# Kernel tuning notes

Hardware: AMD Instinct MI355X
Metric: run time of the kernel (lower is better)

The kernel has to match this reference:

```python
import jax, jax.numpy as jnp
import numpy as np
from jax import lax


def setup_inputs() -> dict:
    key = jax.random.key(0)
    k1, k2 = jax.random.split(key)
    L, B, d = 2048, 16, 1024
    x = jax.random.normal(k1, (L, B, d), dtype=jnp.float32)
    val_range = (3.0 / d) ** 0.5
    weight = jax.random.uniform(k2, (d, 3 * d), dtype=jnp.float32,
                                minval=-val_range, maxval=val_range)
    bias = jnp.zeros((2 * d,), dtype=jnp.float32)
    c0 = jnp.zeros((B, d), dtype=jnp.float32)
    return {"x": x, "weight": weight, "bias": bias, "c0": c0}


def reference(x, weight, bias, c0):
    # x: [L, B, d]; weight: [d, 3d]; bias: [2d]; c0: [B, d]
    L, B, d = x.shape
    u = (x.reshape(-1, d) @ weight).reshape(L, B, d, 3)
    x_tilde = u[..., 0]                               # [L, B, d]
    forget = jax.nn.sigmoid(u[..., 1] + bias[:d])     # [L, B, d]
    reset = jax.nn.sigmoid(u[..., 2] + bias[d:])      # [L, B, d]
    # k == 3 case: x_prime is the raw input (highway connection)
    x_prime = x

    def step(c_prev, ft_xt):
        ft, xt = ft_xt
        c = (c_prev - xt) * ft + xt
        return c, c

    c_last, cs = lax.scan(step, c0, (forget, x_tilde))
    g = jnp.tanh(cs)  # activation_type == 1
    h = (g - x_prime) * reset + x_prime
    return h, c_last
```

## Files before the change

### kernel.cpp

```cpp
#include <hip/hip_runtime.h>

#define L_SEQ 2048
#define BATCH 16
#define DDIM  1024
#define MDIM  (L_SEQ * BATCH)
#define NDIM  (3 * DDIM)
#define KDIM  DDIM
#define CH    (BATCH * DDIM)
#define NSEG  32
#define SEGL  64

typedef __attribute__((ext_vector_type(8))) short short8;
typedef __attribute__((ext_vector_type(4))) float f32x4;

static __device__ __forceinline__ unsigned short f2bf(float f) {
  unsigned int u = __builtin_bit_cast(unsigned int, f);
  unsigned int lsb = (u >> 16) & 1u;
  u += 0x7fffu + lsb;
  return (unsigned short)(u >> 16);
}
static __device__ __forceinline__ float bf2f(unsigned short s) {
  unsigned int u = ((unsigned int)s) << 16;
  return __builtin_bit_cast(float, u);
}

static __device__ __forceinline__ void gll16(const void* g, void* l) {
  __builtin_amdgcn_global_load_lds(
      (const __attribute__((address_space(1))) unsigned int*)g,
      (__attribute__((address_space(3))) unsigned int*)l, 16, 0, 0);
}


__global__ void k_convert_x(const float4* __restrict__ x, ushort4* __restrict__ xb, int n4) {
  int i = blockIdx.x * blockDim.x + threadIdx.x;
  int stride = gridDim.x * blockDim.x;
  for (; i < n4; i += stride) {
    float4 v = x[i];
    ushort4 o;
    o.x = f2bf(v.x); o.y = f2bf(v.y); o.z = f2bf(v.z); o.w = f2bf(v.w);
    xb[i] = o;
  }
}

__global__ void k_convert_w(const float* __restrict__ w, unsigned short* __restrict__ wb) {
  int gid = blockIdx.x * 256 + threadIdx.x;
  int k = gid & (KDIM - 1);
  int n = gid >> 10;
  int col = (n < DDIM) ? 3 * n : (n < 2 * DDIM) ? 3 * (n - DDIM) + 1 : 3 * (n - 2 * DDIM) + 2;
  wb[gid] = f2bf(w[(size_t)k * NDIM + col]);
}


#define MFMA1(I, J, A, B) \
  acc[I][J] = __builtin_amdgcn_mfma_f32_16x16x32_bf16(A, B, acc[I][J], 0, 0, 0);

#define TILE32(T) do {                                                        \
  const char* bufC = LDSc + ((T) & 1) * 16384;                                \
  char*       bufN = LDSc + (((T) + 1) & 1) * 16384;                          \
  const int kb = (((T) + 1) & 31) * 64;                                       \
  gll16(srcA0 + kb, bufN + dstOff);                                           \
  gll16(srcA1 + kb, bufN + 4096 + dstOff);                                    \
  gll16(srcB0 + kb, bufN + 8192 + dstOff);                                    \
  gll16(srcB1 + kb, bufN + 12288 + dstOff);                                   \
  __builtin_amdgcn_sched_barrier(0);                                          \
  a0 = *(const short8*)(bufC + aRd);                                          \
  a1 = *(const short8*)(bufC + aRd + 1024);                                   \
  a2 = *(const short8*)(bufC + aRd + 2048);                                   \
  a3 = *(const short8*)(bufC + aRd + 3072);                                   \
  b0 = *(const short8*)(bufC + 8192 + bRd);                                   \
  b1 = *(const short8*)(bufC + 8192 + bRd + 1024);                            \
  b2 = *(const short8*)(bufC + 8192 + bRd + 2048);                            \
  b3 = *(const short8*)(bufC + 8192 + bRd + 3072);                            \
  MFMA1(0, 0, a0, b0) MFMA1(0, 1, a0, b1) MFMA1(0, 2, a0, b2) MFMA1(0, 3, a0, b3) \
  MFMA1(1, 0, a1, b0) MFMA1(1, 1, a1, b1) MFMA1(1, 2, a1, b2) MFMA1(1, 3, a1, b3) \
  MFMA1(2, 0, a2, b0) MFMA1(2, 1, a2, b1) MFMA1(2, 2, a2, b2) MFMA1(2, 3, a2, b3) \
  MFMA1(3, 0, a3, b0) MFMA1(3, 1, a3, b1) MFMA1(3, 2, a3, b2) MFMA1(3, 3, a3, b3) \
  asm volatile("s_waitcnt vmcnt(0)" ::: "memory");                            \
  __builtin_amdgcn_s_barrier();                                               \
} while (0)

__global__ __launch_bounds__(256, 3) void k_gemm128(
    const unsigned short* __restrict__ xb,
    const unsigned short* __restrict__ wb,
    const float* __restrict__ bias,
    unsigned short* __restrict__ xtb,
    unsigned short* __restrict__ fbuf,
    unsigned short* __restrict__ rbuf) {
  __shared__ char LDS[32768];
  char* LDSc = LDS;

  const int tid  = threadIdx.x;
  const int lane = tid & 63;
  const int wid  = tid >> 6;
  const int wr   = wid >> 1;
  const int wc   = wid & 1;

  int bid = blockIdx.x;
  int wg = (bid & 7) * 768 + (bid >> 3);
  int mt = wg / 24;
  int nt = wg - mt * 24;
  const int rowBase = mt * 128;
  const int colBase = nt * 128;

  const int l15 = lane & 15;
  const int sl  = lane >> 4;
  const int ra0 = wr * 64 + l15;
  const int rb0 = wc * 64 + l15;
  const int aRd = ra0 * 64 + (sl ^ ((ra0 >> 1) & 3)) * 16;
  const int bRd = rb0 * 64 + (sl ^ ((rb0 >> 1) & 3)) * 16;

  const int p0i = tid, p1i = 256 + tid;
  const int r0 = p0i >> 2, r1 = p1i >> 2;
  const int s0 = (p0i & 3) ^ ((r0 >> 1) & 3);
  const int s1 = (p1i & 3) ^ ((r1 >> 1) & 3);
  const char* srcA0 = (const char*)xb + (size_t)(rowBase + r0) * 2048 + s0 * 16;
  const char* srcA1 = (const char*)xb + (size_t)(rowBase + r1) * 2048 + s1 * 16;
  const char* srcB0 = (const char*)wb + (size_t)(colBase + r0) * 2048 + s0 * 16;
  const char* srcB1 = (const char*)wb + (size_t)(colBase + r1) * 2048 + s1 * 16;
  const int dstOff = wid * 1024;

  f32x4 acc[4][4];
#pragma unroll
  for (int ii = 0; ii < 4; ++ii)
#pragma unroll
    for (int jj = 0; jj < 4; ++jj)
      acc[ii][jj] = (f32x4){0.f, 0.f, 0.f, 0.f};

  gll16(srcA0, LDSc + dstOff);
  gll16(srcA1, LDSc + 4096 + dstOff);
  gll16(srcB0, LDSc + 8192 + dstOff);
  gll16(srcB1, LDSc + 12288 + dstOff);
  asm volatile("s_waitcnt vmcnt(0)" ::: "memory");
  __builtin_amdgcn_s_barrier();

  short8 a0, a1, a2, a3;
  short8 b0, b1, b2, b3;

  for (int i = 0; i < 16; ++i) {
    TILE32(2 * i);
    TILE32(2 * i + 1);
  }

  const int region = colBase >> 10;
#pragma unroll
  for (int m = 0; m < 4; ++m) {
    int grow = rowBase + wr * 64 + m * 16 + ((lane >> 4) << 2);
#pragma unroll
    for (int n = 0; n < 4; ++n) {
      int gcol = colBase + wc * 64 + n * 16 + (lane & 15);
      f32x4 v = acc[m][n];
      if (region == 0) {
#pragma unroll
        for (int j = 0; j < 4; ++j)
          xtb[(size_t)(grow + j) * DDIM + gcol] = f2bf(v[j]);
      } else {
        float bv = bias[gcol - DDIM];
        unsigned short* dst = (region == 1) ? fbuf : rbuf;
        int lcol = gcol - (region << 10);
#pragma unroll
        for (int j = 0; j < 4; ++j) {
          float sg = 1.0f / (1.0f + __expf(-(v[j] + bv)));
          dst[(size_t)(grow + j) * DDIM + lcol] = f2bf(sg);
        }
      }
    }
  }
}


__global__ __launch_bounds__(256) void k_scan1(
    const unsigned short* __restrict__ fbuf,
    const unsigned short* __restrict__ xtb,
    float4* __restrict__ AB) {
  int chp = blockIdx.x * 256 + threadIdx.x;
  int seg = blockIdx.y;
  size_t base = (size_t)seg * SEGL * CH + chp * 2;
  const unsigned int* fp = (const unsigned int*)(fbuf + base);
  const unsigned int* xp = (const unsigned int*)(xtb + base);
  float a0 = 1.f, a1 = 1.f, b0 = 0.f, b1 = 0.f;
#pragma unroll 8
  for (int s = 0; s < SEGL; ++s) {
    unsigned int fv = fp[(size_t)s * (CH / 2)];
    unsigned int xv = xp[(size_t)s * (CH / 2)];
    float f0 = bf2f((unsigned short)fv), f1 = bf2f((unsigned short)(fv >> 16));
    float x0 = bf2f((unsigned short)xv), x1 = bf2f((unsigned short)(xv >> 16));
    b0 = (b0 - x0) * f0 + x0;  a0 *= f0;
    b1 = (b1 - x1) * f1 + x1;  a1 *= f1;
  }
  AB[(size_t)seg * (CH / 2) + chp] = (float4){a0, b0, a1, b1};
}


__global__ __launch_bounds__(256) void k_scan2(
    const float* __restrict__ c0,
    const float4* __restrict__ AB,
    float* __restrict__ Cin,
    float* __restrict__ clast) {
  int chp = blockIdx.x * 256 + threadIdx.x;
  float2 cc = ((const float2*)c0)[chp];
  float ca = cc.x, cb = cc.y;
#pragma unroll
  for (int s = 0; s < NSEG; ++s) {
    ((float2*)Cin)[(size_t)s * (CH / 2) + chp] = (float2){ca, cb};
    float4 ab = AB[(size_t)s * (CH / 2) + chp];
    ca = ca * ab.x + ab.y;
    cb = cb * ab.z + ab.w;
  }
  ((float2*)clast)[chp] = (float2){ca, cb};
}


__global__ __launch_bounds__(256) void k_scan3(
    const float* __restrict__ x,
    const unsigned short* __restrict__ fbuf,
    const unsigned short* __restrict__ xtb,
    const unsigned short* __restrict__ rbuf,
    const float* __restrict__ Cin,
    float* __restrict__ h) {
  int chp = blockIdx.x * 256 + threadIdx.x;
  int seg = blockIdx.y;
  float2 cc = ((const float2*)Cin)[(size_t)seg * (CH / 2) + chp];
  float ca = cc.x, cb = cc.y;
  size_t base = (size_t)seg * SEGL * CH + chp * 2;
  const unsigned int* fp = (const unsigned int*)(fbuf + base);
  const unsigned int* tp = (const unsigned int*)(xtb + base);
  const unsigned int* rp = (const unsigned int*)(rbuf + base);
  const float2* xp = (const float2*)(x + base);
  float2* hp = (float2*)(h + base);
#pragma unroll 4
  for (int s = 0; s < SEGL; ++s) {
    unsigned int fv = fp[(size_t)s * (CH / 2)];
    unsigned int tv = tp[(size_t)s * (CH / 2)];
    unsigned int rv = rp[(size_t)s * (CH / 2)];
    float2 xv = xp[(size_t)s * (CH / 2)];
    float f0 = bf2f((unsigned short)fv), f1 = bf2f((unsigned short)(fv >> 16));
    float t0 = bf2f((unsigned short)tv), t1 = bf2f((unsigned short)(tv >> 16));
    float r0 = bf2f((unsigned short)rv), r1 = bf2f((unsigned short)(rv >> 16));
    ca = (ca - t0) * f0 + t0;
    cb = (cb - t1) * f1 + t1;
    float e0 = __expf(-2.f * fabsf(ca));
    float e1 = __expf(-2.f * fabsf(cb));
    float g0 = copysignf((1.f - e0) / (1.f + e0), ca);
    float g1 = copysignf((1.f - e1) / (1.f + e1), cb);
    float h0 = (g0 - xv.x) * r0 + xv.x;
    float h1 = (g1 - xv.y) * r1 + xv.y;
    hp[(size_t)s * (CH / 2)] = (float2){h0, h1};
  }
}


extern "C" void kernel_launch(void* const* d_in, const int* in_sizes, int n_in,
                              void* d_out, int out_size, void* d_ws, size_t ws_size,
                              hipStream_t stream) {
  const float* x    = (const float*)d_in[0];
  const float* w    = (const float*)d_in[1];
  const float* bias = (const float*)d_in[2];
  const float* c0   = (const float*)d_in[3];
  float* out = (float*)d_out;
  char* ws = (char*)d_ws;

  unsigned short* wb   = (unsigned short*)(ws);
  float4*         AB   = (float4*)(ws);
  float*          Cin  = (float*)(ws + 4194304);
  unsigned short* xtb  = (unsigned short*)(ws + 6291456);
  unsigned short* fbuf = (unsigned short*)(ws + 73400320);
  unsigned short* rbuf = (unsigned short*)(ws + 140509184);
  unsigned short* xb = (unsigned short*)d_out;

  k_convert_x<<<2048, 256, 0, stream>>>((const float4*)x, (ushort4*)xb, MDIM * KDIM / 4);
  k_convert_w<<<(NDIM * KDIM) / 256, 256, 0, stream>>>(w, wb);

  k_gemm128<<<6144, 256, 0, stream>>>(xb, wb, bias, xtb, fbuf, rbuf);

  k_scan1<<<dim3(32, NSEG), 256, 0, stream>>>(fbuf, xtb, AB);
  k_scan2<<<32, 256, 0, stream>>>(c0, AB, Cin, out + (size_t)L_SEQ * CH);
  k_scan3<<<dim3(32, NSEG), 256, 0, stream>>>(x, fbuf, xtb, rbuf, Cin, out);
}
```

Before: 463.1 us.

## Enlarge GEMM tile to 256x256 with 32x32 MFMA, quad-buffered LDS, and vectorize scans

Replaces the 128x128 GEMM tile (4 waves, 16x16x32 MFMA, double-buffered LDS) with a 256x256 tile using 8 waves, 32x32x16 MFMA, a 4-stage LDS ring with two K-steps prefetched ahead, and s_setprio around the MFMA block. Larger tiles raise arithmetic intensity and cut global and LDS traffic per FLOP, and the deeper prefetch hides load latency. The cost is 128KB of LDS per block and more registers, which lowers occupancy. The scan kernels now process 8 channels per thread with 16-byte loads, using fewer, wider memory transactions but fewer threads in flight.

```diff
diff --git a/kernel.cpp b/kernel.cpp
--- a/kernel.cpp
+++ b/kernel.cpp
@@ -12,6 +12,7 @@
 
 typedef __attribute__((ext_vector_type(8))) short short8;
 typedef __attribute__((ext_vector_type(4))) float f32x4;
+typedef __attribute__((ext_vector_type(16))) float f32x16;
 
 static __device__ __forceinline__ unsigned short f2bf(float f) {
   unsigned int u = __builtin_bit_cast(unsigned int, f);
@@ -51,116 +52,156 @@
 }
 
 
-#define MFMA1(I, J, A, B) \
-  acc[I][J] = __builtin_amdgcn_mfma_f32_16x16x32_bf16(A, B, acc[I][J], 0, 0, 0);
+#define MFMA32(ACC, A, B) \
+  ACC = __builtin_amdgcn_mfma_f32_32x32x16_bf16(A, B, ACC, 0, 0, 0);
 
 #define TILE32(T) do {                                                        \
-  const char* bufC = LDSc + ((T) & 1) * 16384;                                \
-  char*       bufN = LDSc + (((T) + 1) & 1) * 16384;                          \
-  const int kb = (((T) + 1) & 31) * 64;                                       \
-  gll16(srcA0 + kb, bufN + dstOff);                                           \
-  gll16(srcA1 + kb, bufN + 4096 + dstOff);                                    \
-  gll16(srcB0 + kb, bufN + 8192 + dstOff);                                    \
-  gll16(srcB1 + kb, bufN + 12288 + dstOff);                                   \
+  const char* bufC = LDSc + ((T) & 3) * 32768;                                \
+  char*       bufS = LDSc + (((T) + 2) & 3) * 32768;                          \
+  const int kb = (((T) + 2) & 31) * 64;                                       \
+  gll16(srcA0 + kb, bufS + dstOff);                                           \
+  gll16(srcA1 + kb, bufS + 8192 + dstOff);                                    \
+  gll16(srcB0 + kb, bufS + 16384 + dstOff);                                   \
+  gll16(srcB1 + kb, bufS + 24576 + dstOff);                                   \
   __builtin_amdgcn_sched_barrier(0);                                          \
-  a0 = *(const short8*)(bufC + aRd);                                          \
-  a1 = *(const short8*)(bufC + aRd + 1024);                                   \
-  a2 = *(const short8*)(bufC + aRd + 2048);                                   \
-  a3 = *(const short8*)(bufC + aRd + 3072);                                   \
-  b0 = *(const short8*)(bufC + 8192 + bRd);                                   \
-  b1 = *(const short8*)(bufC + 8192 + bRd + 1024);                            \
-  b2 = *(const short8*)(bufC + 8192 + bRd + 2048);                            \
-  b3 = *(const short8*)(bufC + 8192 + bRd + 3072);                            \
-  MFMA1(0, 0, a0, b0) MFMA1(0, 1, a0, b1) MFMA1(0, 2, a0, b2) MFMA1(0, 3, a0, b3) \
-  MFMA1(1, 0, a1, b0) MFMA1(1, 1, a1, b1) MFMA1(1, 2, a1, b2) MFMA1(1, 3, a1, b3) \
-  MFMA1(2, 0, a2, b0) MFMA1(2, 1, a2, b1) MFMA1(2, 2, a2, b2) MFMA1(2, 3, a2, b3) \
-  MFMA1(3, 0, a3, b0) MFMA1(3, 1, a3, b1) MFMA1(3, 2, a3, b2) MFMA1(3, 3, a3, b3) \
-  asm volatile("s_waitcnt vmcnt(0)" ::: "memory");                            \
+  fa0 = *(const short8*)(bufC + aA00);                                        \
+  fa1 = *(const short8*)(bufC + aA10);                                        \
+  fa2 = *(const short8*)(bufC + aA20);                                        \
+  fa3 = *(const short8*)(bufC + aA30);                                        \
+  fb0 = *(const short8*)(bufC + bA00);                                        \
+  fb1 = *(const short8*)(bufC + bA10);                                        \
+  ga0 = *(const short8*)(bufC + aA01);                                        \
+  ga1 = *(const short8*)(bufC + aA11);                                        \
+  ga2 = *(const short8*)(bufC + aA21);                                        \
+  ga3 = *(const short8*)(bufC + aA31);                                        \
+  gb0 = *(const short8*)(bufC + bA01);                                        \
+  gb1 = *(const short8*)(bufC + bA11);                                        \
+  __builtin_amdgcn_s_setprio(1);                                              \
+  MFMA32(acc[0][0], fa0, fb0) MFMA32(acc[0][1], fa0, fb1)                     \
+  MFMA32(acc[1][0], fa1, fb0) MFMA32(acc[1][1], fa1, fb1)                     \
+  MFMA32(acc[2][0], fa2, fb0) MFMA32(acc[2][1], fa2, fb1)                     \
+  MFMA32(acc[3][0], fa3, fb0) MFMA32(acc[3][1], fa3, fb1)                     \
+  MFMA32(acc[0][0], ga0, gb0) MFMA32(acc[0][1], ga0, gb1)                     \
+  MFMA32(acc[1][0], ga1, gb0) MFMA32(acc[1][1], ga1, gb1)                     \
+  MFMA32(acc[2][0], ga2, gb0) MFMA32(acc[2][1], ga2, gb1)                     \
+  MFMA32(acc[3][0], ga3, gb0) MFMA32(acc[3][1], ga3, gb1)                     \
+  __builtin_amdgcn_s_setprio(0);                                              \
+  asm volatile("s_waitcnt vmcnt(4)" ::: "memory");                            \
   __builtin_amdgcn_s_barrier();                                               \
 } while (0)
 
-__global__ __launch_bounds__(256, 3) void k_gemm128(
+__global__ __launch_bounds__(512, 2) void k_gemm256(
     const unsigned short* __restrict__ xb,
     const unsigned short* __restrict__ wb,
     const float* __restrict__ bias,
     unsigned short* __restrict__ xtb,
     unsigned short* __restrict__ fbuf,
     unsigned short* __restrict__ rbuf) {
-  __shared__ char LDS[32768];
+  __shared__ char LDS[131072];
   char* LDSc = LDS;
 
   const int tid  = threadIdx.x;
   const int lane = tid & 63;
   const int wid  = tid >> 6;
-  const int wr   = wid >> 1;
-  const int wc   = wid & 1;
+  const int wr   = wid >> 2;
+  const int wc   = wid & 3;
 
   int bid = blockIdx.x;
-  int wg = (bid & 7) * 768 + (bid >> 3);
-  int mt = wg / 24;
-  int nt = wg - mt * 24;
-  const int rowBase = mt * 128;
-  const int colBase = nt * 128;
-
-  const int l15 = lane & 15;
-  const int sl  = lane >> 4;
-  const int ra0 = wr * 64 + l15;
-  const int rb0 = wc * 64 + l15;
-  const int aRd = ra0 * 64 + (sl ^ ((ra0 >> 1) & 3)) * 16;
-  const int bRd = rb0 * 64 + (sl ^ ((rb0 >> 1) & 3)) * 16;
-
-  const int p0i = tid, p1i = 256 + tid;
-  const int r0 = p0i >> 2, r1 = p1i >> 2;
-  const int s0 = (p0i & 3) ^ ((r0 >> 1) & 3);
-  const int s1 = (p1i & 3) ^ ((r1 >> 1) & 3);
-  const char* srcA0 = (const char*)xb + (size_t)(rowBase + r0) * 2048 + s0 * 16;
-  const char* srcA1 = (const char*)xb + (size_t)(rowBase + r1) * 2048 + s1 * 16;
-  const char* srcB0 = (const char*)wb + (size_t)(colBase + r0) * 2048 + s0 * 16;
-  const char* srcB1 = (const char*)wb + (size_t)(colBase + r1) * 2048 + s1 * 16;
+  int wg = (bid & 7) * 192 + (bid >> 3);
+  int mt = wg / 12;
+  int nt = wg - mt * 12;
+  const int rowBase = mt * 256;
+  const int colBase = nt * 256;
+
+  const int l31 = lane & 31;
+  const int lh  = lane >> 5;
+  int aA00, aA10, aA20, aA30, aA01, aA11, aA21, aA31;
+  int bA00, bA10, bA01, bA11;
+  {
+    int r0 = wr * 128 + 0 * 32 + l31;
+    int r1 = wr * 128 + 1 * 32 + l31;
+    int r2 = wr * 128 + 2 * 32 + l31;
+    int r3 = wr * 128 + 3 * 32 + l31;
+    aA00 = r0 * 64 + (((lh + 0) ^ ((r0 >> 1) & 3)) << 4);
+    aA10 = r1 * 64 + (((lh + 0) ^ ((r1 >> 1) & 3)) << 4);
+    aA20 = r2 * 64 + (((lh + 0) ^ ((r2 >> 1) & 3)) << 4);
+    aA30 = r3 * 64 + (((lh + 0) ^ ((r3 >> 1) & 3)) << 4);
+    aA01 = r0 * 64 + (((lh + 2) ^ ((r0 >> 1) & 3)) << 4);
+    aA11 = r1 * 64 + (((lh + 2) ^ ((r1 >> 1) & 3)) << 4);
+    aA21 = r2 * 64 + (((lh + 2) ^ ((r2 >> 1) & 3)) << 4);
+    aA31 = r3 * 64 + (((lh + 2) ^ ((r3 >> 1) & 3)) << 4);
+    int c0 = wc * 64 + 0 * 32 + l31;
+    int c1 = wc * 64 + 1 * 32 + l31;
+    bA00 = 16384 + c0 * 64 + (((lh + 0) ^ ((c0 >> 1) & 3)) << 4);
+    bA10 = 16384 + c1 * 64 + (((lh + 0) ^ ((c1 >> 1) & 3)) << 4);
+    bA01 = 16384 + c0 * 64 + (((lh + 2) ^ ((c0 >> 1) & 3)) << 4);
+    bA11 = 16384 + c1 * 64 + (((lh + 2) ^ ((c1 >> 1) & 3)) << 4);
+  }
+
+  const int p0i = tid, p1i = 512 + tid;
+  const int r0s = p0i >> 2, r1s = p1i >> 2;
+  const int s0 = (p0i & 3) ^ ((r0s >> 1) & 3);
+  const int s1 = (p1i & 3) ^ ((r1s >> 1) & 3);
+  const char* srcA0 = (const char*)xb + (size_t)(rowBase + r0s) * 2048 + s0 * 16;
+  const char* srcA1 = (const char*)xb + (size_t)(rowBase + r1s) * 2048 + s1 * 16;
+  const char* srcB0 = (const char*)wb + (size_t)(colBase + r0s) * 2048 + s0 * 16;
+  const char* srcB1 = (const char*)wb + (size_t)(colBase + r1s) * 2048 + s1 * 16;
   const int dstOff = wid * 1024;
 
-  f32x4 acc[4][4];
+  f32x16 acc[4][2];
 #pragma unroll
   for (int ii = 0; ii < 4; ++ii)
 #pragma unroll
-    for (int jj = 0; jj < 4; ++jj)
-      acc[ii][jj] = (f32x4){0.f, 0.f, 0.f, 0.f};
+    for (int jj = 0; jj < 2; ++jj)
+#pragma unroll
+      for (int e = 0; e < 16; ++e)
+        acc[ii][jj][e] = 0.f;
 
   gll16(srcA0, LDSc + dstOff);
-  gll16(srcA1, LDSc + 4096 + dstOff);
-  gll16(srcB0, LDSc + 8192 + dstOff);
-  gll16(srcB1, LDSc + 12288 + dstOff);
+  gll16(srcA1, LDSc + 8192 + dstOff);
+  gll16(srcB0, LDSc + 16384 + dstOff);
+  gll16(srcB1, LDSc + 24576 + dstOff);
+  gll16(srcA0 + 64, LDSc + 32768 + dstOff);
+  gll16(srcA1 + 64, LDSc + 40960 + dstOff);
+  gll16(srcB0 + 64, LDSc + 49152 + dstOff);
+  gll16(srcB1 + 64, LDSc + 57344 + dstOff);
+  asm volatile("s_waitcnt vmcnt(4)" ::: "memory");
+  __builtin_amdgcn_s_barrier();
+
+  short8 fa0, fa1, fa2, fa3, fb0, fb1;
+  short8 ga0, ga1, ga2, ga3, gb0, gb1;
+
+  for (int i = 0; i < 8; ++i) {
+    TILE32(4 * i);
+    TILE32(4 * i + 1);
+    TILE32(4 * i + 2);
+    TILE32(4 * i + 3);
+  }
   asm volatile("s_waitcnt vmcnt(0)" ::: "memory");
-  __builtin_amdgcn_s_barrier();
-
-  short8 a0, a1, a2, a3;
-  short8 b0, b1, b2, b3;
-
-  for (int i = 0; i < 16; ++i) {
-    TILE32(2 * i);
-    TILE32(2 * i + 1);
-  }
 
   const int region = colBase >> 10;
 #pragma unroll
   for (int m = 0; m < 4; ++m) {
-    int grow = rowBase + wr * 64 + m * 16 + ((lane >> 4) << 2);
-#pragma unroll
-    for (int n = 0; n < 4; ++n) {
-      int gcol = colBase + wc * 64 + n * 16 + (lane & 15);
-      f32x4 v = acc[m][n];
+#pragma unroll
+    for (int n = 0; n < 2; ++n) {
+      f32x16 v = acc[m][n];
+      int gcol = colBase + wc * 64 + n * 32 + l31;
+      int growb = rowBase + wr * 128 + m * 32 + 4 * lh;
       if (region == 0) {
 #pragma unroll
-        for (int j = 0; j < 4; ++j)
-          xtb[(size_t)(grow + j) * DDIM + gcol] = f2bf(v[j]);
+        for (int j = 0; j < 16; ++j) {
+          int rr = (j & 3) + 8 * (j >> 2);
+          xtb[(size_t)(growb + rr) * DDIM + gcol] = f2bf(v[j]);
+        }
       } else {
         float bv = bias[gcol - DDIM];
         unsigned short* dst = (region == 1) ? fbuf : rbuf;
         int lcol = gcol - (region << 10);
 #pragma unroll
-        for (int j = 0; j < 4; ++j) {
+        for (int j = 0; j < 16; ++j) {
+          int rr = (j & 3) + 8 * (j >> 2);
           float sg = 1.0f / (1.0f + __expf(-(v[j] + bv)));
-          dst[(size_t)(grow + j) * DDIM + lcol] = f2bf(sg);
+          dst[(size_t)(growb + rr) * DDIM + lcol] = f2bf(sg);
         }
       }
     }
@@ -172,22 +213,32 @@
     const unsigned short* __restrict__ fbuf,
     const unsigned short* __restrict__ xtb,
     float4* __restrict__ AB) {
-  int chp = blockIdx.x * 256 + threadIdx.x;
+  int idx = blockIdx.x * 256 + threadIdx.x;
   int seg = blockIdx.y;
-  size_t base = (size_t)seg * SEGL * CH + chp * 2;
-  const unsigned int* fp = (const unsigned int*)(fbuf + base);
-  const unsigned int* xp = (const unsigned int*)(xtb + base);
-  float a0 = 1.f, a1 = 1.f, b0 = 0.f, b1 = 0.f;
-#pragma unroll 8
+  int pp = idx * 4;
+  size_t base = (size_t)seg * SEGL * CH + (size_t)pp * 2;
+  const uint4* fp = (const uint4*)(fbuf + base);
+  const uint4* xp = (const uint4*)(xtb + base);
+  float a[8], b[8];
+#pragma unroll
+  for (int e = 0; e < 8; ++e) { a[e] = 1.f; b[e] = 0.f; }
+#pragma unroll 4
   for (int s = 0; s < SEGL; ++s) {
-    unsigned int fv = fp[(size_t)s * (CH / 2)];
-    unsigned int xv = xp[(size_t)s * (CH / 2)];
-    float f0 = bf2f((unsigned short)fv), f1 = bf2f((unsigned short)(fv >> 16));
-    float x0 = bf2f((unsigned short)xv), x1 = bf2f((unsigned short)(xv >> 16));
-    b0 = (b0 - x0) * f0 + x0;  a0 *= f0;
-    b1 = (b1 - x1) * f1 + x1;  a1 *= f1;
-  }
-  AB[(size_t)seg * (CH / 2) + chp] = (float4){a0, b0, a1, b1};
+    uint4 fv = fp[(size_t)s * (CH / 8)];
+    uint4 xv = xp[(size_t)s * (CH / 8)];
+    unsigned int fw[4] = {fv.x, fv.y, fv.z, fv.w};
+    unsigned int xw[4] = {xv.x, xv.y, xv.z, xv.w};
+#pragma unroll
+    for (int q = 0; q < 4; ++q) {
+      float f0 = bf2f((unsigned short)fw[q]), f1 = bf2f((unsigned short)(fw[q] >> 16));
+      float x0 = bf2f((unsigned short)xw[q]), x1 = bf2f((unsigned short)(xw[q] >> 16));
+      b[2 * q]     = (b[2 * q] - x0) * f0 + x0;      a[2 * q]     *= f0;
+      b[2 * q + 1] = (b[2 * q + 1] - x1) * f1 + x1;  a[2 * q + 1] *= f1;
+    }
+  }
+#pragma unroll
+  for (int q = 0; q < 4; ++q)
+    AB[(size_t)seg * (CH / 2) + pp + q] = (float4){a[2 * q], b[2 * q], a[2 * q + 1], b[2 * q + 1]};
 }
 
 
@@ -217,34 +268,47 @@
     const unsigned short* __restrict__ rbuf,
     const float* __restrict__ Cin,
     float* __restrict__ h) {
-  int chp = blockIdx.x * 256 + threadIdx.x;
+  int idx = blockIdx.x * 256 + threadIdx.x;
   int seg = blockIdx.y;
-  float2 cc = ((const float2*)Cin)[(size_t)seg * (CH / 2) + chp];
-  float ca = cc.x, cb = cc.y;
-  size_t base = (size_t)seg * SEGL * CH + chp * 2;
-  const unsigned int* fp = (const unsigned int*)(fbuf + base);
-  const unsigned int* tp = (const unsigned int*)(xtb + base);
-  const unsigned int* rp = (const unsigned int*)(rbuf + base);
-  const float2* xp = (const float2*)(x + base);
-  float2* hp = (float2*)(h + base);
-#pragma unroll 4
+  int pp = idx * 4;
+  float4 ci0 = *(const float4*)(Cin + ((size_t)seg * (CH / 2) + pp) * 2);
+  float4 ci1 = *(const float4*)(Cin + ((size_t)seg * (CH / 2) + pp) * 2 + 4);
+  float c[8] = {ci0.x, ci0.y, ci0.z, ci0.w, ci1.x, ci1.y, ci1.z, ci1.w};
+  size_t base = (size_t)seg * SEGL * CH + (size_t)pp * 2;
+  const uint4* fp = (const uint4*)(fbuf + base);
+  const uint4* tp = (const uint4*)(xtb + base);
+  const uint4* rp = (const uint4*)(rbuf + base);
+  const float4* xp = (const float4*)(x + base);
+  float4* hp = (float4*)(h + base);
+#pragma unroll 2
   for (int s = 0; s < SEGL; ++s) {
-    unsigned int fv = fp[(size_t)s * (CH / 2)];
-    unsigned int tv = tp[(size_t)s * (CH / 2)];
-    unsigned int rv = rp[(size_t)s * (CH / 2)];
-    float2 xv = xp[(size_t)s * (CH / 2)];
-    float f0 = bf2f((unsigned short)fv), f1 = bf2f((unsigned short)(fv >> 16));
-    float t0 = bf2f((unsigned short)tv), t1 = bf2f((unsigned short)(tv >> 16));
-    float r0 = bf2f((unsigned short)rv), r1 = bf2f((unsigned short)(rv >> 16));
-    ca = (ca - t0) * f0 + t0;
-    cb = (cb - t1) * f1 + t1;
-    float e0 = __expf(-2.f * fabsf(ca));
-    float e1 = __expf(-2.f * fabsf(cb));
-    float g0 = copysignf((1.f - e0) / (1.f + e0), ca);
-    float g1 = copysignf((1.f - e1) / (1.f + e1), cb);
-    float h0 = (g0 - xv.x) * r0 + xv.x;
-    float h1 = (g1 - xv.y) * r1 + xv.y;
-    hp[(size_t)s * (CH / 2)] = (float2){h0, h1};
+    uint4 fv = fp[(size_t)s * (CH / 8)];
+    uint4 tv = tp[(size_t)s * (CH / 8)];
+    uint4 rv = rp[(size_t)s * (CH / 8)];
+    float4 xv0 = xp[(size_t)s * (CH / 4)];
+    float4 xv1 = xp[(size_t)s * (CH / 4) + 1];
+    unsigned int fw[4] = {fv.x, fv.y, fv.z, fv.w};
+    unsigned int tw[4] = {tv.x, tv.y, tv.z, tv.w};
+    unsigned int rw[4] = {rv.x, rv.y, rv.z, rv.w};
+    float xs[8] = {xv0.x, xv0.y, xv0.z, xv0.w, xv1.x, xv1.y, xv1.z, xv1.w};
+    float hs[8];
+#pragma unroll
+    for (int q = 0; q < 4; ++q) {
+      float f0 = bf2f((unsigned short)fw[q]), f1 = bf2f((unsigned short)(fw[q] >> 16));
+      float t0 = bf2f((unsigned short)tw[q]), t1 = bf2f((unsigned short)(tw[q] >> 16));
+      float r0 = bf2f((unsigned short)rw[q]), r1 = bf2f((unsigned short)(rw[q] >> 16));
+      int e0 = 2 * q, e1 = 2 * q + 1;
+      c[e0] = (c[e0] - t0) * f0 + t0;
+      c[e1] = (c[e1] - t1) * f1 + t1;
+      float q0 = __expf(-2.f * fabsf(c[e0]));
+      float q1 = __expf(-2.f * fabsf(c[e1]));
+      float g0 = copysignf((1.f - q0) / (1.f + q0), c[e0]);
+      float g1 = copysignf((1.f - q1) / (1.f + q1), c[e1]);
+      hs[e0] = (g0 - xs[e0]) * r0 + xs[e0];
+      hs[e1] = (g1 - xs[e1]) * r1 + xs[e1];
+    }
+    hp[(size_t)s * (CH / 4)]     = (float4){hs[0], hs[1], hs[2], hs[3]};
+    hp[(size_t)s * (CH / 4) + 1] = (float4){hs[4], hs[5], hs[6], hs[7]};
   }
 }
 
@@ -270,9 +334,9 @@
   k_convert_x<<<2048, 256, 0, stream>>>((const float4*)x, (ushort4*)xb, MDIM * KDIM / 4);
   k_convert_w<<<(NDIM * KDIM) / 256, 256, 0, stream>>>(w, wb);
 
-  k_gemm128<<<6144, 256, 0, stream>>>(xb, wb, bias, xtb, fbuf, rbuf);
-
-  k_scan1<<<dim3(32, NSEG), 256, 0, stream>>>(fbuf, xtb, AB);
+  k_gemm256<<<1536, 512, 0, stream>>>(xb, wb, bias, xtb, fbuf, rbuf);
+
+  k_scan1<<<dim3(8, NSEG), 256, 0, stream>>>(fbuf, xtb, AB);
   k_scan2<<<32, 256, 0, stream>>>(c0, AB, Cin, out + (size_t)L_SEQ * CH);
-  k_scan3<<<dim3(32, NSEG), 256, 0, stream>>>(x, fbuf, xtb, rbuf, Cin, out);
-}
+  k_scan3<<<dim3(8, NSEG), 256, 0, stream>>>(x, fbuf, xtb, rbuf, Cin, out);
+}
```

New measurement: 468.3 us. About the same (+1.1%).

## Enlarge GEMM block tile to 256x256 with 128x128 per-wave accumulators

Applied to the files above, without the earlier changes.

Replaces the 128x128 block tile GEMM with a 256x256 tile, where each of four waves computes a 128x128 sub-tile using an 8x8 array of MFMA accumulators. The double-buffered LDS grows to 64KB and occupancy is set to one block per CU. The aim is to raise arithmetic intensity per LDS read and global load, cutting memory traffic per FLOP. The cost is heavy register pressure from 256 accumulator floats per lane, possible spilling, lower occupancy that leaves less latency hiding, and fewer blocks (1536), which affects load balance.

```diff
diff --git a/kernel.cpp b/kernel.cpp
--- a/kernel.cpp
+++ b/kernel.cpp
@@ -51,42 +51,14 @@
 }
 
 
-#define MFMA1(I, J, A, B) \
-  acc[I][J] = __builtin_amdgcn_mfma_f32_16x16x32_bf16(A, B, acc[I][J], 0, 0, 0);
-
-#define TILE32(T) do {                                                        \
-  const char* bufC = LDSc + ((T) & 1) * 16384;                                \
-  char*       bufN = LDSc + (((T) + 1) & 1) * 16384;                          \
-  const int kb = (((T) + 1) & 31) * 64;                                       \
-  gll16(srcA0 + kb, bufN + dstOff);                                           \
-  gll16(srcA1 + kb, bufN + 4096 + dstOff);                                    \
-  gll16(srcB0 + kb, bufN + 8192 + dstOff);                                    \
-  gll16(srcB1 + kb, bufN + 12288 + dstOff);                                   \
-  __builtin_amdgcn_sched_barrier(0);                                          \
-  a0 = *(const short8*)(bufC + aRd);                                          \
-  a1 = *(const short8*)(bufC + aRd + 1024);                                   \
-  a2 = *(const short8*)(bufC + aRd + 2048);                                   \
-  a3 = *(const short8*)(bufC + aRd + 3072);                                   \
-  b0 = *(const short8*)(bufC + 8192 + bRd);                                   \
-  b1 = *(const short8*)(bufC + 8192 + bRd + 1024);                            \
-  b2 = *(const short8*)(bufC + 8192 + bRd + 2048);                            \
-  b3 = *(const short8*)(bufC + 8192 + bRd + 3072);                            \
-  MFMA1(0, 0, a0, b0) MFMA1(0, 1, a0, b1) MFMA1(0, 2, a0, b2) MFMA1(0, 3, a0, b3) \
-  MFMA1(1, 0, a1, b0) MFMA1(1, 1, a1, b1) MFMA1(1, 2, a1, b2) MFMA1(1, 3, a1, b3) \
-  MFMA1(2, 0, a2, b0) MFMA1(2, 1, a2, b1) MFMA1(2, 2, a2, b2) MFMA1(2, 3, a2, b3) \
-  MFMA1(3, 0, a3, b0) MFMA1(3, 1, a3, b1) MFMA1(3, 2, a3, b2) MFMA1(3, 3, a3, b3) \
-  asm volatile("s_waitcnt vmcnt(0)" ::: "memory");                            \
-  __builtin_amdgcn_s_barrier();                                               \
-} while (0)
-
-__global__ __launch_bounds__(256, 3) void k_gemm128(
+__global__ __launch_bounds__(256, 1) void k_gemm4w(
     const unsigned short* __restrict__ xb,
     const unsigned short* __restrict__ wb,
     const float* __restrict__ bias,
     unsigned short* __restrict__ xtb,
     unsigned short* __restrict__ fbuf,
     unsigned short* __restrict__ rbuf) {
-  __shared__ char LDS[32768];
+  __shared__ char LDS[65536];
   char* LDSc = LDS;
 
   const int tid  = threadIdx.x;
@@ -96,58 +68,82 @@
   const int wc   = wid & 1;
 
   int bid = blockIdx.x;
-  int wg = (bid & 7) * 768 + (bid >> 3);
-  int mt = wg / 24;
-  int nt = wg - mt * 24;
-  const int rowBase = mt * 128;
-  const int colBase = nt * 128;
+  int wg = (bid & 7) * 192 + (bid >> 3);
+  int mt = wg / 12;
+  int nt = wg - mt * 12;
+  const int rowBase = mt * 256;
+  const int colBase = nt * 256;
 
   const int l15 = lane & 15;
   const int sl  = lane >> 4;
-  const int ra0 = wr * 64 + l15;
-  const int rb0 = wc * 64 + l15;
-  const int aRd = ra0 * 64 + (sl ^ ((ra0 >> 1) & 3)) * 16;
-  const int bRd = rb0 * 64 + (sl ^ ((rb0 >> 1) & 3)) * 16;
-
-  const int p0i = tid, p1i = 256 + tid;
-  const int r0 = p0i >> 2, r1 = p1i >> 2;
-  const int s0 = (p0i & 3) ^ ((r0 >> 1) & 3);
-  const int s1 = (p1i & 3) ^ ((r1 >> 1) & 3);
-  const char* srcA0 = (const char*)xb + (size_t)(rowBase + r0) * 2048 + s0 * 16;
-  const char* srcA1 = (const char*)xb + (size_t)(rowBase + r1) * 2048 + s1 * 16;
-  const char* srcB0 = (const char*)wb + (size_t)(colBase + r0) * 2048 + s0 * 16;
-  const char* srcB1 = (const char*)wb + (size_t)(colBase + r1) * 2048 + s1 * 16;
-  const int dstOff = wid * 1024;
-
-  f32x4 acc[4][4];
-#pragma unroll
-  for (int ii = 0; ii < 4; ++ii)
-#pragma unroll
-    for (int jj = 0; jj < 4; ++jj)
+  int aOff[8], bOff[8];
+#pragma unroll
+  for (int m = 0; m < 8; ++m) {
+    int r = wr * 128 + m * 16 + l15;
+    aOff[m] = r * 64 + ((sl ^ ((r >> 1) & 3)) << 4);
+    int c = wc * 128 + m * 16 + l15;
+    bOff[m] = 16384 + c * 64 + ((sl ^ ((c >> 1) & 3)) << 4);
+  }
+
+  const char* srcA[4];
+  const char* srcB[4];
+#pragma unroll
+  for (int k = 0; k < 4; ++k) {
+    int u = k * 256 + tid;
+    int r = u >> 2;
+    int s = (u & 3) ^ ((r >> 1) & 3);
+    srcA[k] = (const char*)xb + (size_t)(rowBase + r) * 2048 + s * 16;
+    srcB[k] = (const char*)wb + (size_t)(colBase + r) * 2048 + s * 16;
+  }
+  const int dstW = wid * 1024;
+
+  f32x4 acc[8][8];
+#pragma unroll
+  for (int ii = 0; ii < 8; ++ii)
+#pragma unroll
+    for (int jj = 0; jj < 8; ++jj)
       acc[ii][jj] = (f32x4){0.f, 0.f, 0.f, 0.f};
 
-  gll16(srcA0, LDSc + dstOff);
-  gll16(srcA1, LDSc + 4096 + dstOff);
-  gll16(srcB0, LDSc + 8192 + dstOff);
-  gll16(srcB1, LDSc + 12288 + dstOff);
+#pragma unroll
+  for (int k = 0; k < 4; ++k) {
+    gll16(srcA[k], LDSc + k * 4096 + dstW);
+    gll16(srcB[k], LDSc + 16384 + k * 4096 + dstW);
+  }
   asm volatile("s_waitcnt vmcnt(0)" ::: "memory");
   __builtin_amdgcn_s_barrier();
 
-  short8 a0, a1, a2, a3;
-  short8 b0, b1, b2, b3;
-
-  for (int i = 0; i < 16; ++i) {
-    TILE32(2 * i);
-    TILE32(2 * i + 1);
+  for (int t = 0; t < 32; ++t) {
+    const char* bufC = LDSc + (t & 1) * 32768;
+    char* bufS = LDSc + ((t + 1) & 1) * 32768;
+    const int kb = ((t + 1) & 31) * 64;
+#pragma unroll
+    for (int k = 0; k < 4; ++k) {
+      gll16(srcA[k] + kb, bufS + k * 4096 + dstW);
+      gll16(srcB[k] + kb, bufS + 16384 + k * 4096 + dstW);
+    }
+    __builtin_amdgcn_sched_barrier(0);
+    short8 a[8], b[8];
+#pragma unroll
+    for (int n = 0; n < 8; ++n)
+      b[n] = *(const short8*)(bufC + bOff[n]);
+#pragma unroll
+    for (int m = 0; m < 8; ++m) {
+      a[m] = *(const short8*)(bufC + aOff[m]);
+#pragma unroll
+      for (int n = 0; n < 8; ++n)
+        acc[m][n] = __builtin_amdgcn_mfma_f32_16x16x32_bf16(a[m], b[n], acc[m][n], 0, 0, 0);
+    }
+    asm volatile("s_waitcnt vmcnt(0)" ::: "memory");
+    __builtin_amdgcn_s_barrier();
   }
 
   const int region = colBase >> 10;
 #pragma unroll
-  for (int m = 0; m < 4; ++m) {
-    int grow = rowBase + wr * 64 + m * 16 + ((lane >> 4) << 2);
-#pragma unroll
-    for (int n = 0; n < 4; ++n) {
-      int gcol = colBase + wc * 64 + n * 16 + (lane & 15);
+  for (int m = 0; m < 8; ++m) {
+    int grow = rowBase + wr * 128 + m * 16 + (sl << 2);
+#pragma unroll
+    for (int n = 0; n < 8; ++n) {
+      int gcol = colBase + wc * 128 + n * 16 + l15;
       f32x4 v = acc[m][n];
       if (region == 0) {
 #pragma unroll
@@ -270,7 +266,7 @@
   k_convert_x<<<2048, 256, 0, stream>>>((const float4*)x, (ushort4*)xb, MDIM * KDIM / 4);
   k_convert_w<<<(NDIM * KDIM) / 256, 256, 0, stream>>>(w, wb);
 
-  k_gemm128<<<6144, 256, 0, stream>>>(xb, wb, bias, xtb, fbuf, rbuf);
+  k_gemm4w<<<1536, 256, 0, stream>>>(xb, wb, bias, xtb, fbuf, rbuf);
 
   k_scan1<<<dim3(32, NSEG), 256, 0, stream>>>(fbuf, xtb, AB);
   k_scan2<<<32, 256, 0, stream>>>(c0, AB, Cin, out + (size_t)L_SEQ * CH);
```

After: 958.3 us. +107.0%, slower.

## Keep full-K weight panel resident in LDS and stream A via registers

Applied to the files above, without the earlier changes.

The GEMM tile changes from 128x128 to 256x64. The entire 64xK weight panel (128 KB) is loaded into LDS once, while each wave streams its own 64-row A strip through registers into a private LDS region with a two-deep register prefetch. This removes the per-k-step block barriers and the B reloads, and processes K in 128-wide steps. The cost is one block per CU because of the 160 KB of LDS, and more A traffic, since each A row is now re-read for every 64-column tile.

```diff
diff --git a/kernel.cpp b/kernel.cpp
--- a/kernel.cpp
+++ b/kernel.cpp
@@ -51,73 +51,99 @@
 }
 
 
-#define MFMA1(I, J, A, B) \
-  acc[I][J] = __builtin_amdgcn_mfma_f32_16x16x32_bf16(A, B, acc[I][J], 0, 0, 0);
-
-#define TILE32(T) do {                                                        \
-  const char* bufC = LDSc + ((T) & 1) * 16384;                                \
-  char*       bufN = LDSc + (((T) + 1) & 1) * 16384;                          \
-  const int kb = (((T) + 1) & 31) * 64;                                       \
-  gll16(srcA0 + kb, bufN + dstOff);                                           \
-  gll16(srcA1 + kb, bufN + 4096 + dstOff);                                    \
-  gll16(srcB0 + kb, bufN + 8192 + dstOff);                                    \
-  gll16(srcB1 + kb, bufN + 12288 + dstOff);                                   \
-  __builtin_amdgcn_sched_barrier(0);                                          \
-  a0 = *(const short8*)(bufC + aRd);                                          \
-  a1 = *(const short8*)(bufC + aRd + 1024);                                   \
-  a2 = *(const short8*)(bufC + aRd + 2048);                                   \
-  a3 = *(const short8*)(bufC + aRd + 3072);                                   \
-  b0 = *(const short8*)(bufC + 8192 + bRd);                                   \
-  b1 = *(const short8*)(bufC + 8192 + bRd + 1024);                            \
-  b2 = *(const short8*)(bufC + 8192 + bRd + 2048);                            \
-  b3 = *(const short8*)(bufC + 8192 + bRd + 3072);                            \
+#define MFMA1(M, N, A, B) \
+  acc[M][N] = __builtin_amdgcn_mfma_f32_16x16x32_bf16(A, B, acc[M][N], 0, 0, 0);
+
+#define STEP(T, P, Q) do {                                                     \
+  if ((T) <= 13) {                  \
+    P##0 = *(const uint4*)(aSrc + ((T) + 2) * 128);                            \
+    P##1 = *(const uint4*)(aSrc +  16384 + ((T) + 2) * 128);                   \
+    P##2 = *(const uint4*)(aSrc +  32768 + ((T) + 2) * 128);                   \
+    P##3 = *(const uint4*)(aSrc +  49152 + ((T) + 2) * 128);                   \
+    P##4 = *(const uint4*)(aSrc +  65536 + ((T) + 2) * 128);                   \
+    P##5 = *(const uint4*)(aSrc +  81920 + ((T) + 2) * 128);                   \
+    P##6 = *(const uint4*)(aSrc +  98304 + ((T) + 2) * 128);                   \
+    P##7 = *(const uint4*)(aSrc + 114688 + ((T) + 2) * 128);                   \
+  }                                                                            \
+  __builtin_amdgcn_sched_barrier(0);                                           \
+                           \
+  a0 = *(const short8*)(LDSc + aRd0);                                          \
+  a1 = *(const short8*)(LDSc + aRd0 + 2048);                                   \
+  a2 = *(const short8*)(LDSc + aRd0 + 4096);                                   \
+  a3 = *(const short8*)(LDSc + aRd0 + 6144);                                   \
+  a4 = *(const short8*)(LDSc + aRd1);                                          \
+  a5 = *(const short8*)(LDSc + aRd1 + 2048);                                   \
+  a6 = *(const short8*)(LDSc + aRd1 + 4096);                                   \
+  a7 = *(const short8*)(LDSc + aRd1 + 6144);                                   \
+                                        \
+  b0 = *(const short8*)(LDSc + bRd0 + (T) * 8192);                             \
+  b1 = *(const short8*)(LDSc + bRd0 + (T) * 8192 + 2048);                      \
+  b2 = *(const short8*)(LDSc + bRd0 + (T) * 8192 + 4096);                      \
+  b3 = *(const short8*)(LDSc + bRd0 + (T) * 8192 + 6144);                      \
+  b4 = *(const short8*)(LDSc + bRd1 + (T) * 8192);                             \
+  b5 = *(const short8*)(LDSc + bRd1 + (T) * 8192 + 2048);                      \
+  b6 = *(const short8*)(LDSc + bRd1 + (T) * 8192 + 4096);                      \
+  b7 = *(const short8*)(LDSc + bRd1 + (T) * 8192 + 6144);                      \
+  \
+  \
+  if ((T) <= 13)      { asm volatile("s_waitcnt vmcnt(8)" ::: "memory"); }     \
+  else if ((T) == 14) { asm volatile("s_waitcnt vmcnt(0)" ::: "memory"); }     \
+  if ((T) <= 14) {                                                             \
+    *(short8*)(aW)        = *(short8*)&Q##0;                                   \
+    *(short8*)(aW + 1024) = *(short8*)&Q##1;                                   \
+    *(short8*)(aW + 2048) = *(short8*)&Q##2;                                   \
+    *(short8*)(aW + 3072) = *(short8*)&Q##3;                                   \
+    *(short8*)(aW + 4096) = *(short8*)&Q##4;                                   \
+    *(short8*)(aW + 5120) = *(short8*)&Q##5;                                   \
+    *(short8*)(aW + 6144) = *(short8*)&Q##6;                                   \
+    *(short8*)(aW + 7168) = *(short8*)&Q##7;                                   \
+  }                                                                            \
+                                                    \
   MFMA1(0, 0, a0, b0) MFMA1(0, 1, a0, b1) MFMA1(0, 2, a0, b2) MFMA1(0, 3, a0, b3) \
   MFMA1(1, 0, a1, b0) MFMA1(1, 1, a1, b1) MFMA1(1, 2, a1, b2) MFMA1(1, 3, a1, b3) \
   MFMA1(2, 0, a2, b0) MFMA1(2, 1, a2, b1) MFMA1(2, 2, a2, b2) MFMA1(2, 3, a2, b3) \
   MFMA1(3, 0, a3, b0) MFMA1(3, 1, a3, b1) MFMA1(3, 2, a3, b2) MFMA1(3, 3, a3, b3) \
-  asm volatile("s_waitcnt vmcnt(0)" ::: "memory");                            \
-  __builtin_amdgcn_s_barrier();                                               \
+  MFMA1(0, 0, a4, b4) MFMA1(0, 1, a4, b5) MFMA1(0, 2, a4, b6) MFMA1(0, 3, a4, b7) \
+  MFMA1(1, 0, a5, b4) MFMA1(1, 1, a5, b5) MFMA1(1, 2, a5, b6) MFMA1(1, 3, a5, b7) \
+  MFMA1(2, 0, a6, b4) MFMA1(2, 1, a6, b5) MFMA1(2, 2, a6, b6) MFMA1(2, 3, a6, b7) \
+  MFMA1(3, 0, a7, b4) MFMA1(3, 1, a7, b5) MFMA1(3, 2, a7, b6) MFMA1(3, 3, a7, b7) \
 } while (0)
 
-__global__ __launch_bounds__(256, 3) void k_gemm128(
+__global__ __launch_bounds__(256, 1) void k_gemm_nb(
     const unsigned short* __restrict__ xb,
     const unsigned short* __restrict__ wb,
     const float* __restrict__ bias,
     unsigned short* __restrict__ xtb,
     unsigned short* __restrict__ fbuf,
     unsigned short* __restrict__ rbuf) {
-  __shared__ char LDS[32768];
+  __shared__ char LDS[163840];
   char* LDSc = LDS;
 
   const int tid  = threadIdx.x;
   const int lane = tid & 63;
-  const int wid  = tid >> 6;
-  const int wr   = wid >> 1;
-  const int wc   = wid & 1;
+  const int wv   = tid >> 6;
 
   int bid = blockIdx.x;
   int wg = (bid & 7) * 768 + (bid >> 3);
-  int mt = wg / 24;
-  int nt = wg - mt * 24;
-  const int rowBase = mt * 128;
-  const int colBase = nt * 128;
+  int mt = wg / 48;
+  int nt = wg - mt * 48;
+  const int rowBase = mt * 256;
+  const int colBase = nt * 64;
 
   const int l15 = lane & 15;
   const int sl  = lane >> 4;
-  const int ra0 = wr * 64 + l15;
-  const int rb0 = wc * 64 + l15;
-  const int aRd = ra0 * 64 + (sl ^ ((ra0 >> 1) & 3)) * 16;
-  const int bRd = rb0 * 64 + (sl ^ ((rb0 >> 1) & 3)) * 16;
-
-  const int p0i = tid, p1i = 256 + tid;
-  const int r0 = p0i >> 2, r1 = p1i >> 2;
-  const int s0 = (p0i & 3) ^ ((r0 >> 1) & 3);
-  const int s1 = (p1i & 3) ^ ((r1 >> 1) & 3);
-  const char* srcA0 = (const char*)xb + (size_t)(rowBase + r0) * 2048 + s0 * 16;
-  const char* srcA1 = (const char*)xb + (size_t)(rowBase + r1) * 2048 + s1 * 16;
-  const char* srcB0 = (const char*)wb + (size_t)(colBase + r0) * 2048 + s0 * 16;
-  const char* srcB1 = (const char*)wb + (size_t)(colBase + r1) * 2048 + s1 * 16;
-  const int dstOff = wid * 1024;
+  const int l7  = lane & 7;
+  const int lr3 = lane >> 3;
+
+  const int fr0 = ((sl)     ^ (l15 & 7)) << 4;
+  const int fr1 = ((4 + sl) ^ (l15 & 7)) << 4;
+  const int aRd0 = wv * 8192 + l15 * 128 + fr0;
+  const int aRd1 = wv * 8192 + l15 * 128 + fr1;
+  const int bRd0 = 32768 + l15 * 128 + fr0;
+  const int bRd1 = 32768 + l15 * 128 + fr1;
+
+  const char* aSrc = (const char*)xb + (size_t)(rowBase + wv * 64 + lr3) * 2048 + l7 * 16;
+  char* aW = LDSc + wv * 8192 + lr3 * 128 + ((l7 ^ lr3) << 4);
 
   f32x4 acc[4][4];
 #pragma unroll
@@ -126,28 +152,64 @@
     for (int jj = 0; jj < 4; ++jj)
       acc[ii][jj] = (f32x4){0.f, 0.f, 0.f, 0.f};
 
-  gll16(srcA0, LDSc + dstOff);
-  gll16(srcA1, LDSc + 4096 + dstOff);
-  gll16(srcB0, LDSc + 8192 + dstOff);
-  gll16(srcB1, LDSc + 12288 + dstOff);
-  asm volatile("s_waitcnt vmcnt(0)" ::: "memory");
+#pragma unroll
+  for (int j = 0; j < 32; ++j) {
+    int u16 = j * 256 + tid;
+    int byteo = u16 << 4;
+    int kb  = byteo >> 13;
+    int loc = byteo & 8191;
+    int r   = loc >> 7;
+    int sp  = (loc >> 4) & 7;
+    const char* src = (const char*)wb + (size_t)(colBase + r) * 2048 + kb * 128 + ((sp ^ (r & 7)) << 4);
+    gll16(src, LDSc + 32768 + (j << 12) + (wv << 10));
+  }
+
+  uint4 p0, p1, p2, p3, p4, p5, p6, p7;
+  uint4 q0, q1, q2, q3, q4, q5, q6, q7;
+
+  p0 = *(const uint4*)(aSrc);
+  p1 = *(const uint4*)(aSrc + 16384);
+  p2 = *(const uint4*)(aSrc + 32768);
+  p3 = *(const uint4*)(aSrc + 49152);
+  p4 = *(const uint4*)(aSrc + 65536);
+  p5 = *(const uint4*)(aSrc + 81920);
+  p6 = *(const uint4*)(aSrc + 98304);
+  p7 = *(const uint4*)(aSrc + 114688);
+  q0 = *(const uint4*)(aSrc + 128);
+  q1 = *(const uint4*)(aSrc + 16384 + 128);
+  q2 = *(const uint4*)(aSrc + 32768 + 128);
+  q3 = *(const uint4*)(aSrc + 49152 + 128);
+  q4 = *(const uint4*)(aSrc + 65536 + 128);
+  q5 = *(const uint4*)(aSrc + 81920 + 128);
+  q6 = *(const uint4*)(aSrc + 98304 + 128);
+  q7 = *(const uint4*)(aSrc + 114688 + 128);
+  asm volatile("s_waitcnt vmcnt(16)" ::: "memory");
   __builtin_amdgcn_s_barrier();
-
-  short8 a0, a1, a2, a3;
-  short8 b0, b1, b2, b3;
-
-  for (int i = 0; i < 16; ++i) {
-    TILE32(2 * i);
-    TILE32(2 * i + 1);
-  }
+  asm volatile("s_waitcnt vmcnt(8)" ::: "memory");
+  *(short8*)(aW)        = *(short8*)&p0;
+  *(short8*)(aW + 1024) = *(short8*)&p1;
+  *(short8*)(aW + 2048) = *(short8*)&p2;
+  *(short8*)(aW + 3072) = *(short8*)&p3;
+  *(short8*)(aW + 4096) = *(short8*)&p4;
+  *(short8*)(aW + 5120) = *(short8*)&p5;
+  *(short8*)(aW + 6144) = *(short8*)&p6;
+  *(short8*)(aW + 7168) = *(short8*)&p7;
+
+  short8 a0, a1, a2, a3, a4, a5, a6, a7;
+  short8 b0, b1, b2, b3, b4, b5, b6, b7;
+
+  STEP(0, p, q);  STEP(1, q, p);  STEP(2, p, q);  STEP(3, q, p);
+  STEP(4, p, q);  STEP(5, q, p);  STEP(6, p, q);  STEP(7, q, p);
+  STEP(8, p, q);  STEP(9, q, p);  STEP(10, p, q); STEP(11, q, p);
+  STEP(12, p, q); STEP(13, q, p); STEP(14, p, q); STEP(15, q, p);
 
   const int region = colBase >> 10;
 #pragma unroll
   for (int m = 0; m < 4; ++m) {
-    int grow = rowBase + wr * 64 + m * 16 + ((lane >> 4) << 2);
+    int grow = rowBase + wv * 64 + m * 16 + (sl << 2);
 #pragma unroll
     for (int n = 0; n < 4; ++n) {
-      int gcol = colBase + wc * 64 + n * 16 + (lane & 15);
+      int gcol = colBase + n * 16 + l15;
       f32x4 v = acc[m][n];
       if (region == 0) {
 #pragma unroll
@@ -190,7 +252,6 @@
   AB[(size_t)seg * (CH / 2) + chp] = (float4){a0, b0, a1, b1};
 }
 
-
 __global__ __launch_bounds__(256) void k_scan2(
     const float* __restrict__ c0,
     const float4* __restrict__ AB,
@@ -208,7 +269,6 @@
   }
   ((float2*)clast)[chp] = (float2){ca, cb};
 }
-
 
 __global__ __launch_bounds__(256) void k_scan3(
     const float* __restrict__ x,
@@ -270,7 +330,7 @@
   k_convert_x<<<2048, 256, 0, stream>>>((const float4*)x, (ushort4*)xb, MDIM * KDIM / 4);
   k_convert_w<<<(NDIM * KDIM) / 256, 256, 0, stream>>>(w, wb);
 
-  k_gemm128<<<6144, 256, 0, stream>>>(xb, wb, bias, xtb, fbuf, rbuf);
+  k_gemm_nb<<<6144, 256, 0, stream>>>(xb, wb, bias, xtb, fbuf, rbuf);
 
   k_scan1<<<dim3(32, NSEG), 256, 0, stream>>>(fbuf, xtb, AB);
   k_scan2<<<32, 256, 0, stream>>>(c0, AB, Cin, out + (size_t)L_SEQ * CH);
```

After: 536.3 us. 1.16x slower.
